# Kernel tuning notes

Measured on AMD Instinct MI355X. Metric: run time of the kernel, lower is better.

Reference implementation:

```python
import jax, jax.numpy as jnp
import numpy as np


def setup_inputs() -> dict:
    key = jax.random.key(0)
    ks = jax.random.split(key, 9)
    B, T, S, D = 4, 256, 256, 512
    scale = 1.0 / np.sqrt(D)
    inp = {
        "output": jax.random.normal(ks[0], (B, T, D), dtype=jnp.float32),
        "context": jax.random.normal(ks[1], (B, S, D), dtype=jnp.float32),
        "mask": jax.random.randint(ks[2], (B, S), 0, 2, dtype=jnp.int32),
        # learned params (nn.Linear stores y = x @ W.T + b; we store W.T directly)
        "Wq": jax.random.normal(ks[3], (D, D), dtype=jnp.float32) * scale,
        "bq": jax.random.normal(ks[4], (D,), dtype=jnp.float32) * scale,
        "Wc": jax.random.normal(ks[5], (D, D), dtype=jnp.float32) * scale,
        "v": jax.random.normal(ks[6], (D,), dtype=jnp.float32) * scale,
        "Wout": jax.random.normal(ks[7], (2 * D, D), dtype=jnp.float32) * scale,
        "bout": jax.random.normal(ks[8], (D,), dtype=jnp.float32) * scale,
    }
    return inp


def reference(output, context, mask, Wq, bq, Wc, v, Wout, bout):
    # output: (B, T, D) decoder states; context: (B, S, D) encoder states
    wq = jnp.einsum("btd,de->bte", output, Wq) + bq          # (B, T, D)
    uh = jnp.einsum("bsd,de->bse", context, Wc)               # (B, S, D)
    # additive score: v . tanh(wq + uh), broadcast over (T, S)
    wquh = jnp.tanh(wq[:, :, None, :] + uh[:, None, :, :])    # (B, T, S, D)
    score = jnp.einsum("btsd,d->bts", wquh, v)                # (B, T, S)
    # masked softmax exactly as the torch code: max over ALL positions,
    # then zero out masked entries (mask==1 means masked) and renormalize.
    max_by_row = jnp.max(score, axis=-1, keepdims=True)
    keep = (1.0 - mask.astype(score.dtype))[:, None, :]       # (B, 1, S)
    attn = jnp.exp(score - max_by_row) * keep
    attn = attn / jnp.sum(attn, axis=-1, keepdims=True)       # (B, T, S)
    mix = jnp.einsum("bts,bsd->btd", attn, context)           # (B, T, D)
    combined = jnp.concatenate([mix, output], axis=-1)        # (B, T, 2D)
    out = jnp.einsum("btf,fd->btd", combined, Wout) + bout    # (B, T, D)
    return out, attn
```

## Files before the change

kernel.cpp:

```cpp
#include <hip/hip_runtime.h>
#include <hip/hip_bf16.h>

#define B_ 4
#define T_ 256
#define S_ 256
#define D_ 512
#define TB 2

typedef __bf16 bf16x8 __attribute__((ext_vector_type(8)));
typedef float  floatx4 __attribute__((ext_vector_type(4)));

#define C2F 2.885390081777926f

static __device__ __forceinline__ unsigned short f2bf(float x) {
    __hip_bfloat16 h = __float2bfloat16(x);
    return *reinterpret_cast<unsigned short*>(&h);
}
static __device__ __forceinline__ float asf(unsigned int u) {
    float f; __builtin_memcpy(&f, &u, 4); return f;
}

struct G4 {
    const float* A;
    const float* W;
    int krow0;
    const float* aux;
    void* C;
    int mode;
};

__global__ __launch_bounds__(1024, 8) void gemm4(G4 g0, G4 g1, G4 g2, G4 g3)
{
    const int tid = threadIdx.x;
    const int bid = blockIdx.x;

    const int z  = bid & 3;
    const int n0 = ((bid >> 2) & 7) * 64;
    const int m0 = (bid >> 5) * 64;

    G4 g = (z == 0) ? g0 : (z == 1) ? g1 : (z == 2) ? g2 : g3;

    __shared__ unsigned short Af[4 * 64 * 8];
    __shared__ unsigned short Bf[4 * 64 * 8];

    const int am = tid >> 4;
    const int ak = (tid & 15) * 2;
    const int bn = tid & 63;
    const int bk = (tid >> 6) * 2;

    const float* Aptr = g.A + (size_t)(m0 + am) * 512 + ak;
    const float* Wptr = g.W + (size_t)(g.krow0 + bk) * 512 + n0 + bn;

    unsigned int* Awr = (unsigned int*)&Af[((am >> 4) * 64
                          + ((am & 15) | ((ak >> 3) << 4))) * 8 + (ak & 7)];
    unsigned int* Bwr = (unsigned int*)&Bf[((bn >> 4) * 64
                          + ((bn & 15) | ((bk >> 3) << 4))) * 8 + (bk & 7)];

    const int wave = tid >> 6, lane = tid & 63;
    const int l15 = lane & 15, quad = lane >> 4;
    const int mf = wave >> 2, nf = wave & 3;
    const unsigned short* Ard = &Af[(mf * 64 + lane) * 8];
    const unsigned short* Brd = &Bf[(nf * 64 + lane) * 8];

    floatx4 acc = (floatx4){0.f, 0.f, 0.f, 0.f};

    for (int chunk = 0; chunk < 16; ++chunk) {
        const int k0 = chunk * 32;
        float2 av = *(const float2*)(Aptr + k0);
        float  b0 = Wptr[(size_t)k0 * 512];
        float  b1 = Wptr[(size_t)k0 * 512 + 512];

        __syncthreads();
        *Awr = (unsigned)f2bf(av.x) | ((unsigned)f2bf(av.y) << 16);
        *Bwr = (unsigned)f2bf(b0)   | ((unsigned)f2bf(b1)   << 16);
        __syncthreads();

        bf16x8 fa = *(const bf16x8*)Ard;
        bf16x8 fb = *(const bf16x8*)Brd;
        acc = __builtin_amdgcn_mfma_f32_16x16x32_bf16(fa, fb, acc, 0, 0, 0);
    }

    const int col = n0 + nf * 16 + l15;
    const int rbase = m0 + mf * 16 + quad * 4;
    if (g.mode == 3) {
        unsigned short* Cb = (unsigned short*)g.C;
        #pragma unroll
        for (int r = 0; r < 4; ++r) {
            int row = rbase + r, bb = row >> 8, ss = row & 255;
            Cb[((size_t)(bb * 64 + (col >> 3)) * 256 + ss) * 8 + (col & 7)]
                = f2bf(C2F * acc[r]);
        }
    } else if (g.mode == 5) {
        unsigned short* Cb = (unsigned short*)g.C;
        #pragma unroll
        for (int r = 0; r < 4; ++r)
            Cb[(size_t)(rbase + r) * 512 + col] = f2bf(acc[r]);
    } else {
        float* Cf = (float*)g.C;
        float bv = g.aux ? g.aux[col] : 0.0f;
        #pragma unroll
        for (int r = 0; r < 4; ++r) {
            float val = acc[r] + bv;
            if (g.mode == 1) val *= C2F;
            Cf[(size_t)(rbase + r) * 512 + col] = val;
        }
    }
}

__global__ __launch_bounds__(1024) void attn_fused(
    const float* __restrict__ wqs,
    const unsigned short* __restrict__ uhb,
    const unsigned short* __restrict__ CWb,
    const float* __restrict__ OB,
    const int*   __restrict__ mask,
    const float* __restrict__ v,
    float* __restrict__ attn_out,
    float* __restrict__ out)
{
    const int bg  = blockIdx.x;
    const int b   = bg / (T_ / TB);
    const int t0  = (bg % (T_ / TB)) * TB;
    const int tid = threadIdx.x;
    const int s   = tid & 255;
    const int h   = tid >> 8;

    __shared__ float  w_s[TB][D_];
    __shared__ float  v_s[D_];
    __shared__ float2 part[4][256];
    __shared__ float2 wred[4];
    __shared__ float  a_s[TB][256];
    __shared__ float  mixp[4][TB][D_];

    if (tid < 512) {
        w_s[0][tid] = wqs[(size_t)(b * T_ + t0 + 0) * D_ + tid];
        w_s[1][tid] = wqs[(size_t)(b * T_ + t0 + 1) * D_ + tid];
        v_s[tid]    = v[tid];
    }
    __syncthreads();

    float acc0 = 0.f, acc1 = 0.f;
    const int dd0 = h * 16;
    const uint4* u4 = (const uint4*)(uhb + ((size_t)(b * 64 + dd0) * 256 + s) * 8);

    #pragma unroll 4
    for (int dd = 0; dd < 16; ++dd) {
        uint4 uu = u4[(size_t)dd * 256];
        float uf[8];
        uf[0] = asf(uu.x << 16); uf[1] = asf(uu.x & 0xffff0000u);
        uf[2] = asf(uu.y << 16); uf[3] = asf(uu.y & 0xffff0000u);
        uf[4] = asf(uu.z << 16); uf[5] = asf(uu.z & 0xffff0000u);
        uf[6] = asf(uu.w << 16); uf[7] = asf(uu.w & 0xffff0000u);

        const int dbase = (dd0 + dd) * 8;
        #pragma unroll
        for (int j = 0; j < 8; ++j) {
            float vv = v_s[dbase + j];
            float x0 = w_s[0][dbase + j] + uf[j];
            float x1 = w_s[1][dbase + j] + uf[j];
            float r0 = __builtin_amdgcn_rcpf(__builtin_amdgcn_exp2f(x0) + 1.0f);
            float r1 = __builtin_amdgcn_rcpf(__builtin_amdgcn_exp2f(x1) + 1.0f);
            acc0 = fmaf(vv, r0, acc0);
            acc1 = fmaf(vv, r1, acc1);
        }
    }
    part[h][s] = make_float2(acc0, acc1);
    __syncthreads();

    float p0 = 0.f, p1 = 0.f;
    if (tid < 256) {
        float A0 = part[0][tid].x + part[1][tid].x + part[2][tid].x + part[3][tid].x;
        float A1 = part[0][tid].y + part[1][tid].y + part[2][tid].y + part[3][tid].y;
        float keep = 1.0f - (float)mask[b * S_ + tid];
        p0 = __builtin_amdgcn_exp2f(-C2F * A0) * keep;
        p1 = __builtin_amdgcn_exp2f(-C2F * A1) * keep;
        float s0 = p0, s1 = p1;
        #pragma unroll
        for (int off = 1; off < 64; off <<= 1) {
            s0 += __shfl_xor(s0, off);
            s1 += __shfl_xor(s1, off);
        }
        if ((tid & 63) == 0) wred[tid >> 6] = make_float2(s0, s1);
    }
    __syncthreads();

    if (tid < 256) {
        float den0 = wred[0].x + wred[1].x + wred[2].x + wred[3].x;
        float den1 = wred[0].y + wred[1].y + wred[2].y + wred[3].y;
        float a0 = p0 * __builtin_amdgcn_rcpf(den0);
        float a1 = p1 * __builtin_amdgcn_rcpf(den1);
        attn_out[(size_t)(b * T_ + t0 + 0) * S_ + tid] = a0;
        attn_out[(size_t)(b * T_ + t0 + 1) * S_ + tid] = a1;
        a_s[0][tid] = a0;
        a_s[1][tid] = a1;
    }
    __syncthreads();

    const int d2 = tid & 255;
    const int sh = h * 64;
    const unsigned short* cw = CWb + ((size_t)(b * S_) + sh) * D_ + 2 * d2;
    float m[TB][2] = {};
    #pragma unroll 8
    for (int s2 = 0; s2 < 64; ++s2) {
        unsigned int cc = *(const unsigned int*)(cw + (size_t)s2 * D_);
        float c0 = asf(cc << 16), c1 = asf(cc & 0xffff0000u);
        #pragma unroll
        for (int t = 0; t < TB; ++t) {
            float a = a_s[t][sh + s2];
            m[t][0] = fmaf(a, c0, m[t][0]);
            m[t][1] = fmaf(a, c1, m[t][1]);
        }
    }
    #pragma unroll
    for (int t = 0; t < TB; ++t) {
        mixp[h][t][2 * d2]     = m[t][0];
        mixp[h][t][2 * d2 + 1] = m[t][1];
    }
    __syncthreads();

    {
        const int t = tid >> 9, d = tid & 511;
        size_t idx = (size_t)(b * T_ + t0 + t) * D_ + d;
        out[idx] = mixp[0][t][d] + mixp[1][t][d] + mixp[2][t][d] + mixp[3][t][d]
                 + OB[idx];
    }
}

extern "C" void kernel_launch(void* const* d_in, const int* in_sizes, int n_in,
                              void* d_out, int out_size, void* d_ws, size_t ws_size,
                              hipStream_t stream) {
    const float* output  = (const float*)d_in[0];
    const float* context = (const float*)d_in[1];
    const int*   mask    = (const int*)d_in[2];
    const float* Wq      = (const float*)d_in[3];
    const float* bq      = (const float*)d_in[4];
    const float* Wc      = (const float*)d_in[5];
    const float* v       = (const float*)d_in[6];
    const float* Wout    = (const float*)d_in[7];
    const float* bout    = (const float*)d_in[8];

    float* out  = (float*)d_out;
    float* attn = out + (size_t)B_ * T_ * D_;

    char* ws = (char*)d_ws;
    float* wqs          = (float*)ws;
    float* OB           = (float*)(ws + (2u << 20));
    unsigned short* uhb = (unsigned short*)(ws + (4u << 20));
    unsigned short* CWb = (unsigned short*)(ws + (5u << 20));

    G4 gwq = { output,  Wq,     0, bq,      wqs, 1 };
    G4 guh = { context, Wc,     0, nullptr, uhb, 3 };
    G4 gob = { output,  Wout, 512, bout,    OB,  4 };
    G4 gcw = { context, Wout,   0, nullptr, CWb, 5 };
    gemm4<<<dim3(512), dim3(1024), 0, stream>>>(gwq, guh, gob, gcw);

    attn_fused<<<dim3(B_ * T_ / TB), dim3(1024), 0, stream>>>(
        wqs, uhb, CWb, OB, mask, v, attn, out);
}
```

Before: 123.7 us.

## Merge GEMM and attention kernels into one persistent kernel with grid barrier

Fuses the two launches into a single 512-block kernel. A global atomic barrier separates the GEMM phase from the attention phase, so the second kernel launch and its gap go away. The attention loop also prefetches the next uh vector one step ahead. This needs a memset before the kernel to reset the barrier counter, and it relies on all 512 blocks of 1024 threads being resident at once, or the kernel deadlocks. The shared-memory footprint grows because both phases' buffers are declared together.

```diff
diff --git a/kernel.cpp b/kernel.cpp
--- a/kernel.cpp
+++ b/kernel.cpp
@@ -11,6 +11,7 @@
 typedef float  floatx4 __attribute__((ext_vector_type(4)));
 
 #define C2F 2.885390081777926f
+#define NBLK 512u
 
 static __device__ __forceinline__ unsigned short f2bf(float x) {
     __hip_bfloat16 h = __float2bfloat16(x);
@@ -20,110 +21,23 @@
     float f; __builtin_memcpy(&f, &u, 4); return f;
 }
 
-struct G4 {
-    const float* A;
-    const float* W;
-    int krow0;
-    const float* aux;
-    void* C;
-    int mode;
+struct MP {
+    const float* output; const float* context; const int* mask;
+    const float* Wq; const float* bq; const float* Wc; const float* v;
+    const float* Wout; const float* bout;
+    float* attn_out; float* out;
+    float* wqs; float* OB;
+    unsigned short* uhb; unsigned short* CWb;
+    unsigned int* bar;
 };
 
-__global__ __launch_bounds__(1024, 8) void gemm4(G4 g0, G4 g1, G4 g2, G4 g3)
+__global__ __launch_bounds__(1024, 8) void mega(MP P)
 {
     const int tid = threadIdx.x;
     const int bid = blockIdx.x;
 
-    const int z  = bid & 3;
-    const int n0 = ((bid >> 2) & 7) * 64;
-    const int m0 = (bid >> 5) * 64;
-
-    G4 g = (z == 0) ? g0 : (z == 1) ? g1 : (z == 2) ? g2 : g3;
-
     __shared__ unsigned short Af[4 * 64 * 8];
     __shared__ unsigned short Bf[4 * 64 * 8];
-
-    const int am = tid >> 4;
-    const int ak = (tid & 15) * 2;
-    const int bn = tid & 63;
-    const int bk = (tid >> 6) * 2;
-
-    const float* Aptr = g.A + (size_t)(m0 + am) * 512 + ak;
-    const float* Wptr = g.W + (size_t)(g.krow0 + bk) * 512 + n0 + bn;
-
-    unsigned int* Awr = (unsigned int*)&Af[((am >> 4) * 64
-                          + ((am & 15) | ((ak >> 3) << 4))) * 8 + (ak & 7)];
-    unsigned int* Bwr = (unsigned int*)&Bf[((bn >> 4) * 64
-                          + ((bn & 15) | ((bk >> 3) << 4))) * 8 + (bk & 7)];
-
-    const int wave = tid >> 6, lane = tid & 63;
-    const int l15 = lane & 15, quad = lane >> 4;
-    const int mf = wave >> 2, nf = wave & 3;
-    const unsigned short* Ard = &Af[(mf * 64 + lane) * 8];
-    const unsigned short* Brd = &Bf[(nf * 64 + lane) * 8];
-
-    floatx4 acc = (floatx4){0.f, 0.f, 0.f, 0.f};
-
-    for (int chunk = 0; chunk < 16; ++chunk) {
-        const int k0 = chunk * 32;
-        float2 av = *(const float2*)(Aptr + k0);
-        float  b0 = Wptr[(size_t)k0 * 512];
-        float  b1 = Wptr[(size_t)k0 * 512 + 512];
-
-        __syncthreads();
-        *Awr = (unsigned)f2bf(av.x) | ((unsigned)f2bf(av.y) << 16);
-        *Bwr = (unsigned)f2bf(b0)   | ((unsigned)f2bf(b1)   << 16);
-        __syncthreads();
-
-        bf16x8 fa = *(const bf16x8*)Ard;
-        bf16x8 fb = *(const bf16x8*)Brd;
-        acc = __builtin_amdgcn_mfma_f32_16x16x32_bf16(fa, fb, acc, 0, 0, 0);
-    }
-
-    const int col = n0 + nf * 16 + l15;
-    const int rbase = m0 + mf * 16 + quad * 4;
-    if (g.mode == 3) {
-        unsigned short* Cb = (unsigned short*)g.C;
-        #pragma unroll
-        for (int r = 0; r < 4; ++r) {
-            int row = rbase + r, bb = row >> 8, ss = row & 255;
-            Cb[((size_t)(bb * 64 + (col >> 3)) * 256 + ss) * 8 + (col & 7)]
-                = f2bf(C2F * acc[r]);
-        }
-    } else if (g.mode == 5) {
-        unsigned short* Cb = (unsigned short*)g.C;
-        #pragma unroll
-        for (int r = 0; r < 4; ++r)
-            Cb[(size_t)(rbase + r) * 512 + col] = f2bf(acc[r]);
-    } else {
-        float* Cf = (float*)g.C;
-        float bv = g.aux ? g.aux[col] : 0.0f;
-        #pragma unroll
-        for (int r = 0; r < 4; ++r) {
-            float val = acc[r] + bv;
-            if (g.mode == 1) val *= C2F;
-            Cf[(size_t)(rbase + r) * 512 + col] = val;
-        }
-    }
-}
-
-__global__ __launch_bounds__(1024) void attn_fused(
-    const float* __restrict__ wqs,
-    const unsigned short* __restrict__ uhb,
-    const unsigned short* __restrict__ CWb,
-    const float* __restrict__ OB,
-    const int*   __restrict__ mask,
-    const float* __restrict__ v,
-    float* __restrict__ attn_out,
-    float* __restrict__ out)
-{
-    const int bg  = blockIdx.x;
-    const int b   = bg / (T_ / TB);
-    const int t0  = (bg % (T_ / TB)) * TB;
-    const int tid = threadIdx.x;
-    const int s   = tid & 255;
-    const int h   = tid >> 8;
-
     __shared__ float  w_s[TB][D_];
     __shared__ float  v_s[D_];
     __shared__ float2 part[4][256];
@@ -131,128 +45,218 @@
     __shared__ float  a_s[TB][256];
     __shared__ float  mixp[4][TB][D_];
 
-    if (tid < 512) {
-        w_s[0][tid] = wqs[(size_t)(b * T_ + t0 + 0) * D_ + tid];
-        w_s[1][tid] = wqs[(size_t)(b * T_ + t0 + 1) * D_ + tid];
-        v_s[tid]    = v[tid];
+    {
+        const int z  = bid & 3;
+        const int n0 = ((bid >> 2) & 7) * 64;
+        const int m0 = (bid >> 5) * 64;
+
+        const float* A; const float* W; const float* aux; int krow0, mode;
+        if      (z == 0) { A = P.output;  W = P.Wq;   aux = P.bq;    krow0 = 0;   mode = 1; }
+        else if (z == 1) { A = P.context; W = P.Wc;   aux = nullptr; krow0 = 0;   mode = 3; }
+        else if (z == 2) { A = P.output;  W = P.Wout; aux = P.bout;  krow0 = 512; mode = 4; }
+        else             { A = P.context; W = P.Wout; aux = nullptr; krow0 = 0;   mode = 5; }
+
+        const int am = tid >> 4;
+        const int ak = (tid & 15) * 2;
+        const int bn = tid & 63;
+        const int bk = (tid >> 6) * 2;
+
+        const float* Aptr = A + (size_t)(m0 + am) * 512 + ak;
+        const float* Wptr = W + (size_t)(krow0 + bk) * 512 + n0 + bn;
+
+        unsigned int* Awr = (unsigned int*)&Af[((am >> 4) * 64
+                              + ((am & 15) | ((ak >> 3) << 4))) * 8 + (ak & 7)];
+        unsigned int* Bwr = (unsigned int*)&Bf[((bn >> 4) * 64
+                              + ((bn & 15) | ((bk >> 3) << 4))) * 8 + (bk & 7)];
+
+        const int wave = tid >> 6, lane = tid & 63;
+        const int l15 = lane & 15, quad = lane >> 4;
+        const int mf = wave >> 2, nf = wave & 3;
+        const unsigned short* Ard = &Af[(mf * 64 + lane) * 8];
+        const unsigned short* Brd = &Bf[(nf * 64 + lane) * 8];
+
+        floatx4 acc = (floatx4){0.f, 0.f, 0.f, 0.f};
+
+        for (int chunk = 0; chunk < 16; ++chunk) {
+            const int k0 = chunk * 32;
+            float2 av = *(const float2*)(Aptr + k0);
+            float  b0 = Wptr[(size_t)k0 * 512];
+            float  b1 = Wptr[(size_t)k0 * 512 + 512];
+
+            __syncthreads();
+            *Awr = (unsigned)f2bf(av.x) | ((unsigned)f2bf(av.y) << 16);
+            *Bwr = (unsigned)f2bf(b0)   | ((unsigned)f2bf(b1)   << 16);
+            __syncthreads();
+
+            bf16x8 fa = *(const bf16x8*)Ard;
+            bf16x8 fb = *(const bf16x8*)Brd;
+            acc = __builtin_amdgcn_mfma_f32_16x16x32_bf16(fa, fb, acc, 0, 0, 0);
+        }
+
+        const int col = n0 + nf * 16 + l15;
+        const int rbase = m0 + mf * 16 + quad * 4;
+        if (mode == 3) {
+            #pragma unroll
+            for (int r = 0; r < 4; ++r) {
+                int row = rbase + r, bb = row >> 8, ss = row & 255;
+                P.uhb[((size_t)(bb * 64 + (col >> 3)) * 256 + ss) * 8 + (col & 7)]
+                    = f2bf(C2F * acc[r]);
+            }
+        } else if (mode == 5) {
+            #pragma unroll
+            for (int r = 0; r < 4; ++r)
+                P.CWb[(size_t)(rbase + r) * 512 + col] = f2bf(acc[r]);
+        } else {
+            float* Cf = (mode == 1) ? P.wqs : P.OB;
+            float bv = aux ? aux[col] : 0.0f;
+            #pragma unroll
+            for (int r = 0; r < 4; ++r) {
+                float val = acc[r] + bv;
+                if (mode == 1) val *= C2F;
+                Cf[(size_t)(rbase + r) * 512 + col] = val;
+            }
+        }
+    }
+
+    __syncthreads();
+    if (tid == 0) {
+        __threadfence();
+        atomicAdd(P.bar, 1u);
+        while (__hip_atomic_load(P.bar, __ATOMIC_ACQUIRE,
+                                 __HIP_MEMORY_SCOPE_AGENT) < NBLK) { }
     }
     __syncthreads();
 
-    float acc0 = 0.f, acc1 = 0.f;
-    const int dd0 = h * 16;
-    const uint4* u4 = (const uint4*)(uhb + ((size_t)(b * 64 + dd0) * 256 + s) * 8);
-
-    #pragma unroll 4
-    for (int dd = 0; dd < 16; ++dd) {
-        uint4 uu = u4[(size_t)dd * 256];
-        float uf[8];
-        uf[0] = asf(uu.x << 16); uf[1] = asf(uu.x & 0xffff0000u);
-        uf[2] = asf(uu.y << 16); uf[3] = asf(uu.y & 0xffff0000u);
-        uf[4] = asf(uu.z << 16); uf[5] = asf(uu.z & 0xffff0000u);
-        uf[6] = asf(uu.w << 16); uf[7] = asf(uu.w & 0xffff0000u);
-
-        const int dbase = (dd0 + dd) * 8;
-        #pragma unroll
-        for (int j = 0; j < 8; ++j) {
-            float vv = v_s[dbase + j];
-            float x0 = w_s[0][dbase + j] + uf[j];
-            float x1 = w_s[1][dbase + j] + uf[j];
-            float r0 = __builtin_amdgcn_rcpf(__builtin_amdgcn_exp2f(x0) + 1.0f);
-            float r1 = __builtin_amdgcn_rcpf(__builtin_amdgcn_exp2f(x1) + 1.0f);
-            acc0 = fmaf(vv, r0, acc0);
-            acc1 = fmaf(vv, r1, acc1);
-        }
-    }
-    part[h][s] = make_float2(acc0, acc1);
-    __syncthreads();
-
-    float p0 = 0.f, p1 = 0.f;
-    if (tid < 256) {
-        float A0 = part[0][tid].x + part[1][tid].x + part[2][tid].x + part[3][tid].x;
-        float A1 = part[0][tid].y + part[1][tid].y + part[2][tid].y + part[3][tid].y;
-        float keep = 1.0f - (float)mask[b * S_ + tid];
-        p0 = __builtin_amdgcn_exp2f(-C2F * A0) * keep;
-        p1 = __builtin_amdgcn_exp2f(-C2F * A1) * keep;
-        float s0 = p0, s1 = p1;
-        #pragma unroll
-        for (int off = 1; off < 64; off <<= 1) {
-            s0 += __shfl_xor(s0, off);
-            s1 += __shfl_xor(s1, off);
-        }
-        if ((tid & 63) == 0) wred[tid >> 6] = make_float2(s0, s1);
-    }
-    __syncthreads();
-
-    if (tid < 256) {
-        float den0 = wred[0].x + wred[1].x + wred[2].x + wred[3].x;
-        float den1 = wred[0].y + wred[1].y + wred[2].y + wred[3].y;
-        float a0 = p0 * __builtin_amdgcn_rcpf(den0);
-        float a1 = p1 * __builtin_amdgcn_rcpf(den1);
-        attn_out[(size_t)(b * T_ + t0 + 0) * S_ + tid] = a0;
-        attn_out[(size_t)(b * T_ + t0 + 1) * S_ + tid] = a1;
-        a_s[0][tid] = a0;
-        a_s[1][tid] = a1;
-    }
-    __syncthreads();
-
-    const int d2 = tid & 255;
-    const int sh = h * 64;
-    const unsigned short* cw = CWb + ((size_t)(b * S_) + sh) * D_ + 2 * d2;
-    float m[TB][2] = {};
-    #pragma unroll 8
-    for (int s2 = 0; s2 < 64; ++s2) {
-        unsigned int cc = *(const unsigned int*)(cw + (size_t)s2 * D_);
-        float c0 = asf(cc << 16), c1 = asf(cc & 0xffff0000u);
+    {
+        const int bg  = bid;
+        const int b   = bg / (T_ / TB);
+        const int t0  = (bg % (T_ / TB)) * TB;
+        const int s   = tid & 255;
+        const int h   = tid >> 8;
+
+        if (tid < 512) {
+            w_s[0][tid] = P.wqs[(size_t)(b * T_ + t0 + 0) * D_ + tid];
+            w_s[1][tid] = P.wqs[(size_t)(b * T_ + t0 + 1) * D_ + tid];
+            v_s[tid]    = P.v[tid];
+        }
+        __syncthreads();
+
+        float acc0 = 0.f, acc1 = 0.f;
+        const int dd0 = h * 16;
+        const uint4* u4 = (const uint4*)(P.uhb + ((size_t)(b * 64 + dd0) * 256 + s) * 8);
+
+        uint4 uu = u4[0];
+        #pragma unroll 4
+        for (int dd = 0; dd < 16; ++dd) {
+            uint4 cur = uu;
+            if (dd < 15) uu = u4[(size_t)(dd + 1) * 256];
+            float uf[8];
+            uf[0] = asf(cur.x << 16); uf[1] = asf(cur.x & 0xffff0000u);
+            uf[2] = asf(cur.y << 16); uf[3] = asf(cur.y & 0xffff0000u);
+            uf[4] = asf(cur.z << 16); uf[5] = asf(cur.z & 0xffff0000u);
+            uf[6] = asf(cur.w << 16); uf[7] = asf(cur.w & 0xffff0000u);
+
+            const int dbase = (dd0 + dd) * 8;
+            #pragma unroll
+            for (int j = 0; j < 8; ++j) {
+                float vv = v_s[dbase + j];
+                float x0 = w_s[0][dbase + j] + uf[j];
+                float x1 = w_s[1][dbase + j] + uf[j];
+                float r0 = __builtin_amdgcn_rcpf(__builtin_amdgcn_exp2f(x0) + 1.0f);
+                float r1 = __builtin_amdgcn_rcpf(__builtin_amdgcn_exp2f(x1) + 1.0f);
+                acc0 = fmaf(vv, r0, acc0);
+                acc1 = fmaf(vv, r1, acc1);
+            }
+        }
+        part[h][s] = make_float2(acc0, acc1);
+        __syncthreads();
+
+        float p0 = 0.f, p1 = 0.f;
+        if (tid < 256) {
+            float A0 = part[0][tid].x + part[1][tid].x + part[2][tid].x + part[3][tid].x;
+            float A1 = part[0][tid].y + part[1][tid].y + part[2][tid].y + part[3][tid].y;
+            float keep = 1.0f - (float)P.mask[b * S_ + tid];
+            p0 = __builtin_amdgcn_exp2f(-C2F * A0) * keep;
+            p1 = __builtin_amdgcn_exp2f(-C2F * A1) * keep;
+            float s0 = p0, s1 = p1;
+            #pragma unroll
+            for (int off = 1; off < 64; off <<= 1) {
+                s0 += __shfl_xor(s0, off);
+                s1 += __shfl_xor(s1, off);
+            }
+            if ((tid & 63) == 0) wred[tid >> 6] = make_float2(s0, s1);
+        }
+        __syncthreads();
+
+        if (tid < 256) {
+            float den0 = wred[0].x + wred[1].x + wred[2].x + wred[3].x;
+            float den1 = wred[0].y + wred[1].y + wred[2].y + wred[3].y;
+            float a0 = p0 * __builtin_amdgcn_rcpf(den0);
+            float a1 = p1 * __builtin_amdgcn_rcpf(den1);
+            P.attn_out[(size_t)(b * T_ + t0 + 0) * S_ + tid] = a0;
+            P.attn_out[(size_t)(b * T_ + t0 + 1) * S_ + tid] = a1;
+            a_s[0][tid] = a0;
+            a_s[1][tid] = a1;
+        }
+        __syncthreads();
+
+        const int d2 = tid & 255;
+        const int sh = h * 64;
+        const unsigned short* cw = P.CWb + ((size_t)(b * S_) + sh) * D_ + 2 * d2;
+        float m[TB][2] = {};
+        #pragma unroll 8
+        for (int s2 = 0; s2 < 64; ++s2) {
+            unsigned int cc = *(const unsigned int*)(cw + (size_t)s2 * D_);
+            float c0 = asf(cc << 16), c1 = asf(cc & 0xffff0000u);
+            #pragma unroll
+            for (int t = 0; t < TB; ++t) {
+                float a = a_s[t][sh + s2];
+                m[t][0] = fmaf(a, c0, m[t][0]);
+                m[t][1] = fmaf(a, c1, m[t][1]);
+            }
+        }
         #pragma unroll
         for (int t = 0; t < TB; ++t) {
-            float a = a_s[t][sh + s2];
-            m[t][0] = fmaf(a, c0, m[t][0]);
-            m[t][1] = fmaf(a, c1, m[t][1]);
-        }
-    }
-    #pragma unroll
-    for (int t = 0; t < TB; ++t) {
-        mixp[h][t][2 * d2]     = m[t][0];
-        mixp[h][t][2 * d2 + 1] = m[t][1];
-    }
-    __syncthreads();
-
-    {
-        const int t = tid >> 9, d = tid & 511;
-        size_t idx = (size_t)(b * T_ + t0 + t) * D_ + d;
-        out[idx] = mixp[0][t][d] + mixp[1][t][d] + mixp[2][t][d] + mixp[3][t][d]
-                 + OB[idx];
+            mixp[h][t][2 * d2]     = m[t][0];
+            mixp[h][t][2 * d2 + 1] = m[t][1];
+        }
+        __syncthreads();
+
+        {
+            const int t = tid >> 9, d = tid & 511;
+            size_t idx = (size_t)(b * T_ + t0 + t) * D_ + d;
+            P.out[idx] = mixp[0][t][d] + mixp[1][t][d] + mixp[2][t][d]
+                       + mixp[3][t][d] + P.OB[idx];
+        }
     }
 }
 
 extern "C" void kernel_launch(void* const* d_in, const int* in_sizes, int n_in,
                               void* d_out, int out_size, void* d_ws, size_t ws_size,
                               hipStream_t stream) {
-    const float* output  = (const float*)d_in[0];
-    const float* context = (const float*)d_in[1];
-    const int*   mask    = (const int*)d_in[2];
-    const float* Wq      = (const float*)d_in[3];
-    const float* bq      = (const float*)d_in[4];
-    const float* Wc      = (const float*)d_in[5];
-    const float* v       = (const float*)d_in[6];
-    const float* Wout    = (const float*)d_in[7];
-    const float* bout    = (const float*)d_in[8];
-
     float* out  = (float*)d_out;
     float* attn = out + (size_t)B_ * T_ * D_;
 
     char* ws = (char*)d_ws;
-    float* wqs          = (float*)ws;
-    float* OB           = (float*)(ws + (2u << 20));
-    unsigned short* uhb = (unsigned short*)(ws + (4u << 20));
-    unsigned short* CWb = (unsigned short*)(ws + (5u << 20));
-
-    G4 gwq = { output,  Wq,     0, bq,      wqs, 1 };
-    G4 guh = { context, Wc,     0, nullptr, uhb, 3 };
-    G4 gob = { output,  Wout, 512, bout,    OB,  4 };
-    G4 gcw = { context, Wout,   0, nullptr, CWb, 5 };
-    gemm4<<<dim3(512), dim3(1024), 0, stream>>>(gwq, guh, gob, gcw);
-
-    attn_fused<<<dim3(B_ * T_ / TB), dim3(1024), 0, stream>>>(
-        wqs, uhb, CWb, OB, mask, v, attn, out);
-}
+    MP P;
+    P.output  = (const float*)d_in[0];
+    P.context = (const float*)d_in[1];
+    P.mask    = (const int*)d_in[2];
+    P.Wq      = (const float*)d_in[3];
+    P.bq      = (const float*)d_in[4];
+    P.Wc      = (const float*)d_in[5];
+    P.v       = (const float*)d_in[6];
+    P.Wout    = (const float*)d_in[7];
+    P.bout    = (const float*)d_in[8];
+    P.attn_out = attn;
+    P.out      = out;
+    P.wqs = (float*)ws;
+    P.OB  = (float*)(ws + (2u << 20));
+    P.uhb = (unsigned short*)(ws + (4u << 20));
+    P.CWb = (unsigned short*)(ws + (5u << 20));
+    P.bar = (unsigned int*)(ws + (10u << 20));
+
+    hipMemsetAsync(P.bar, 0, sizeof(unsigned int), stream);
+
+    mega<<<dim3(NBLK), dim3(1024), 0, stream>>>(P);
+}
```

After: 257.5 us. 108% more time.
